# Optimization experiments

Measured on AMD Instinct MI355X. Metric: run time of the kernel, lower is better.

Reference implementation:

```python
import jax, jax.numpy as jnp
import numpy as np

N_SRC = 50000
N_DST = 50000
E = 400000
D_IN = 256
D_OUT = 256


def setup_inputs() -> dict:
    key = jax.random.key(0)
    k1, k2, k3, k4, k5 = jax.random.split(key, 5)
    src_feats = jax.random.normal(k1, (N_SRC, D_IN), dtype=jnp.float32)
    edge_feats = jax.random.normal(k2, (E, D_IN), dtype=jnp.float32)
    src_idx = jax.random.randint(k3, (E,), 0, N_SRC, dtype=jnp.int32)
    dst_idx = jax.random.randint(k4, (E,), 0, N_DST, dtype=jnp.int32)
    # xavier_uniform over [2*in_feat, out_feat] (transposed init in torch, same bound)
    fan_in, fan_out = 2 * D_IN, D_OUT
    bound = np.sqrt(6.0 / (fan_in + fan_out))
    weights = jax.random.uniform(k5, (2 * D_IN, D_OUT), dtype=jnp.float32,
                                 minval=-bound, maxval=bound)
    h_bias = jnp.zeros((D_OUT,), dtype=jnp.float32)
    return {"src_feats": src_feats, "edge_feats": edge_feats,
            "src_idx": src_idx, "dst_idx": dst_idx,
            "weights": weights, "h_bias": h_bias, "num_dst": N_DST}


def reference(src_feats, edge_feats, src_idx, dst_idx, weights, h_bias, num_dst):
    # edge_feat_mp_op == 'concat':
    #   m = concat([src_h, e_h], -1) @ W  ==  src_h @ W[:D] + e_h @ W[D:]
    d = src_feats.shape[1]
    m = src_feats[src_idx] @ weights[:d] + edge_feats @ weights[d:]  # [E, D_OUT]
    # in-degree normalization: norm = in_deg(dst)^{-0.5}, applied per edge (e_mul_v)
    deg = jax.ops.segment_sum(jnp.ones((m.shape[0],), jnp.float32), dst_idx,
                              num_segments=num_dst)
    norm = jnp.where(deg > 0, jax.lax.rsqrt(jnp.maximum(deg, 1.0)), 0.0)
    h = jax.ops.segment_sum(m * norm[dst_idx][:, None], dst_idx,
                            num_segments=num_dst)  # [N_DST, D_OUT]
    return h + h_bias
```

## Files before the change

### kernel.cpp

```cpp
#include <hip/hip_runtime.h>

typedef __attribute__((ext_vector_type(8))) short bf16x8;
typedef __attribute__((ext_vector_type(4))) float f32x4;

#define D_IN 256
#define D_OUT 256
#define KDIM 512
#define GM 64
#define G_ROWS 8
#define CHUNK 2
#define IDCAP 128
#define SCAN_BLOCKS 256

static __device__ __forceinline__ unsigned short f2bf(float f) {
    union { float f; unsigned int u; } x; x.f = f;
    unsigned int r = (x.u + 0x7FFFu + ((x.u >> 16) & 1u)) >> 16;
    return (unsigned short)r;
}

#define GLOAD16(gp, lp) __builtin_amdgcn_global_load_lds(                    \
    (const __attribute__((address_space(1))) void*)(gp),                     \
    (__attribute__((address_space(3))) void*)(lp), 16, 0, 0)

__global__ void zero_wfrag_kernel(int* __restrict__ deg, int n, int zblocks,
                                  const float* __restrict__ W, unsigned short* __restrict__ wf) {
    int b = blockIdx.x;
    if (b < zblocks) {
        int i = b * 256 + threadIdx.x;
        if (i < n) deg[i] = 0;
    } else {
        int t = (b - zblocks) * 256 + threadIdx.x;
        if (t < 16 * 16 * 64) {
            int l  = t & 63;
            int kk = (t >> 6) & 15;
            int nt = t >> 10;
            int c  = nt * 16 + (l & 15);
            int kb = kk * 32 + (l >> 4) * 8;
            union { unsigned short u[8]; uint4 v; } pk;
#pragma unroll
            for (int j = 0; j < 8; ++j) pk.u[j] = f2bf(W[(size_t)(kb + j) * D_OUT + c]);
            *reinterpret_cast<uint4*>(&wf[(size_t)t * 8]) = pk.v;
        }
    }
}

__global__ void count_kernel(const int* __restrict__ dst, int* __restrict__ deg, int E) {
    int e = blockIdx.x * 256 + threadIdx.x;
    if (e < E) atomicAdd(&deg[dst[e]], 1);
}

__global__ void scan_part_kernel(const int* __restrict__ deg, int* __restrict__ part, int n) {
    __shared__ int red[256];
    int b = blockIdx.x, t = threadIdx.x;
    int per = (n + SCAN_BLOCKS - 1) / SCAN_BLOCKS;
    int lo = b * per;
    int hi = lo + per; if (hi > n) hi = n;
    int s = 0;
    for (int i = lo + t; i < hi; i += 256) s += deg[i];
    red[t] = s;
    __syncthreads();
    for (int o = 128; o > 0; o >>= 1) {
        if (t < o) red[t] += red[t + o];
        __syncthreads();
    }
    if (t == 0) part[b] = red[0];
}

__global__ void scan_emit_kernel(const int* __restrict__ deg, const int* __restrict__ part,
                                 int* __restrict__ offsets, int* __restrict__ cursor,
                                 float* __restrict__ norm, int n) {
    int b = blockIdx.x, t = threadIdx.x;
    int per = (n + SCAN_BLOCKS - 1) / SCAN_BLOCKS;
    int lo = b * per;
    int hi = lo + per; if (hi > n) hi = n;
    int v = 0;
    for (int i = t; i < b; i += 64) v += part[i];
#pragma unroll
    for (int o = 32; o > 0; o >>= 1) v += __shfl_down(v, o);
    int base = __shfl(v, 0);
    int sub = (per + 63) / 64;
    int llo = lo + t * sub;
    int lhi = llo + sub;
    if (lhi > hi) lhi = hi;
    if (llo > hi) llo = hi;
    int s = 0;
    for (int i = llo; i < lhi; ++i) s += deg[i];
    int incl = s;
#pragma unroll
    for (int o = 1; o < 64; o <<= 1) { int u = __shfl_up(incl, o); if (t >= o) incl += u; }
    int run = base + incl - s;
    for (int i = llo; i < lhi; ++i) {
        int d = deg[i];
        offsets[i] = run; cursor[i] = run;
        norm[i] = (d > 0) ? rsqrtf((float)d) : 0.0f;
        run += d;
    }
    if (b == SCAN_BLOCKS - 1 && t == 63) offsets[n] = base + incl;
}

__global__ void scatter_kernel(const int* __restrict__ dst, const int* __restrict__ src_idx,
                               int* __restrict__ cursor, int2* __restrict__ rec, int E) {
    int e = blockIdx.x * 256 + threadIdx.x;
    if (e < E) {
        int p = atomicAdd(&cursor[dst[e]], 1);
        rec[p] = make_int2(e, src_idx[e]);
    }
}

__global__ __launch_bounds__(256) void agg_kernel(
    const float* __restrict__ src_feats,
    const float* __restrict__ edge_feats,
    const int2* __restrict__ rec,
    const int* __restrict__ offsets,
    unsigned short* __restrict__ agg,
    int n_dst)
{
    __shared__ __align__(16) float fb[4][2][CHUNK][KDIM];
    __shared__ __align__(16) int2 idb[4][IDCAP + 128];

    const int wv = threadIdx.x >> 6;
    const int ln = threadIdx.x & 63;
    const int rowbase = (blockIdx.x * 4 + wv) * G_ROWS;

    int off_l;
    {
        int k = (ln <= G_ROWS) ? ln : G_ROWS;
        int i = rowbase + k;
        if (i > n_dst) i = n_dst;
        off_l = offsets[i];
    }
    const int s  = __shfl(off_l, 0);
    const int nE = __shfl(off_l, G_ROWS) - s;

    float4 a0 = make_float4(0.f, 0.f, 0.f, 0.f);
    float4 a1 = make_float4(0.f, 0.f, 0.f, 0.f);
    int curRow = 0;
    int curEnd = __shfl(off_l, 1) - s;

    auto flush = [&]() {
        int gr = rowbase + curRow;
        if (gr < n_dst) {
            ushort4 p0, p1;
            p0.x = f2bf(a0.x); p0.y = f2bf(a0.y); p0.z = f2bf(a0.z); p0.w = f2bf(a0.w);
            p1.x = f2bf(a1.x); p1.y = f2bf(a1.y); p1.z = f2bf(a1.z); p1.w = f2bf(a1.w);
            *reinterpret_cast<ushort4*>(&agg[(size_t)gr * KDIM + ln * 4]) = p0;
            *reinterpret_cast<ushort4*>(&agg[(size_t)gr * KDIM + D_IN + ln * 4]) = p1;
        }
        a0 = make_float4(0.f, 0.f, 0.f, 0.f);
        a1 = make_float4(0.f, 0.f, 0.f, 0.f);
    };

    for (int g0 = 0; g0 < nE; g0 += IDCAP) {
        int segN = nE - g0; if (segN > IDCAP) segN = IDCAP;
        const int sg = s + g0;
        const int base16 = sg & ~1;
        const int extra = sg - base16;
        const int idops = ((segN + extra) * 8 + 1023) >> 10;
        for (int o = 0; o < idops; ++o)
            GLOAD16((const char*)(rec + base16) + o * 1024 + ln * 16,
                    (char*)&idb[wv][0] + o * 1024);
        asm volatile("s_waitcnt vmcnt(0)" ::: "memory");
        __builtin_amdgcn_sched_barrier(0);

        const int nCh = (segN + CHUNK - 1) / CHUNK;

        auto issue = [&](int ci) {
            int buf = ci & 1;
            int e0 = ci * CHUNK;
#pragma unroll
            for (int t = 0; t < CHUNK; ++t) {
                int j = e0 + t;
                int sid = 0, eid = 0;
                if (j < segN) { int2 v = idb[wv][j + extra]; eid = v.x; sid = v.y; }
                float* lp = &fb[wv][buf][t][0];
                GLOAD16(src_feats  + (size_t)sid * D_IN + ln * 4, lp);
                GLOAD16(edge_feats + (size_t)eid * D_IN + ln * 4, lp + D_IN);
            }
        };

        issue(0); issue(1);
        for (int ci = 0; ci < nCh; ++ci) {
            asm volatile("s_waitcnt vmcnt(4)" ::: "memory");
            __builtin_amdgcn_sched_barrier(0);
            int buf = ci & 1;
            int e0 = ci * CHUNK;
#pragma unroll
            for (int t = 0; t < CHUNK; ++t) {
                int j = e0 + t;
                if (j >= segN) break;
                int ja = g0 + j;
                while (ja >= curEnd) {
                    flush();
                    ++curRow;
                    curEnd = __shfl(off_l, curRow + 1) - s;
                }
                float4 v0 = *reinterpret_cast<const float4*>(&fb[wv][buf][t][ln * 4]);
                float4 v1 = *reinterpret_cast<const float4*>(&fb[wv][buf][t][D_IN + ln * 4]);
                a0.x += v0.x; a0.y += v0.y; a0.z += v0.z; a0.w += v0.w;
                a1.x += v1.x; a1.y += v1.y; a1.z += v1.z; a1.w += v1.w;
            }
            issue(ci + 2);
        }
        asm volatile("s_waitcnt vmcnt(0)" ::: "memory");
        __builtin_amdgcn_sched_barrier(0);
    }
    while (curRow < G_ROWS) { flush(); ++curRow; }
}

__global__ __launch_bounds__(256) void gemm_kernel(
    const unsigned short* __restrict__ agg,
    const unsigned short* __restrict__ wfrag,
    const float* __restrict__ norm,
    const float* __restrict__ bias,
    float* __restrict__ out,
    int n_dst)
{
    __shared__ __align__(16) unsigned short As[GM * KDIM];

    const int wv = threadIdx.x >> 6;
    const int ln = threadIdx.x & 63;
    const int lrow = ln & 15;
    const int lgrp = ln >> 4;
    const int base = blockIdx.x * GM;

    for (int r = wv; r < GM; r += 4) {
        int gr = base + r; if (gr >= n_dst) gr = n_dst - 1;
        GLOAD16(agg + (size_t)gr * KDIM + (size_t)((ln ^ (r & 7)) * 8),
                (char*)As + r * 1024);
    }
    asm volatile("s_waitcnt vmcnt(0)" ::: "memory");
    __syncthreads();

    f32x4 acc[4][4];
#pragma unroll
    for (int m = 0; m < 4; ++m)
#pragma unroll
        for (int n = 0; n < 4; ++n) acc[m][n] = (f32x4)(0.0f);

#pragma unroll
    for (int kk = 0; kk < 16; ++kk) {
        bf16x8 A[4];
#pragma unroll
        for (int m = 0; m < 4; ++m) {
            int r = m * 16 + lrow;
            int g = (kk * 4 + lgrp) ^ (r & 7);
            A[m] = *reinterpret_cast<const bf16x8*>((const char*)As + r * 1024 + g * 16);
        }
#pragma unroll
        for (int n = 0; n < 4; ++n) {
            int nt = wv * 4 + n;
            bf16x8 B = *reinterpret_cast<const bf16x8*>(&wfrag[(((size_t)nt * 16 + kk) * 64 + ln) * 8]);
#pragma unroll
            for (int m = 0; m < 4; ++m)
                acc[m][n] = __builtin_amdgcn_mfma_f32_16x16x32_bf16(A[m], B, acc[m][n], 0, 0, 0);
        }
    }

    float bias_r[4];
#pragma unroll
    for (int n = 0; n < 4; ++n) bias_r[n] = bias[wv * 64 + n * 16 + lrow];

#pragma unroll
    for (int m = 0; m < 4; ++m) {
#pragma unroll
        for (int j = 0; j < 4; ++j) {
            int r = base + m * 16 + lgrp * 4 + j;
            if (r < n_dst) {
                float nv = norm[r];
#pragma unroll
                for (int n = 0; n < 4; ++n)
                    out[(size_t)r * D_OUT + wv * 64 + n * 16 + lrow] = acc[m][n][j] * nv + bias_r[n];
            }
        }
    }
}

extern "C" void kernel_launch(void* const* d_in, const int* in_sizes, int n_in,
                              void* d_out, int out_size, void* d_ws, size_t ws_size,
                              hipStream_t stream) {
    const float* src_feats  = (const float*)d_in[0];
    const float* edge_feats = (const float*)d_in[1];
    const int*   src_idx    = (const int*)d_in[2];
    const int*   dst_idx    = (const int*)d_in[3];
    const float* weights    = (const float*)d_in[4];
    const float* h_bias     = (const float*)d_in[5];

    const int E     = in_sizes[2];
    const int n_dst = out_size / D_OUT;
    float* out = (float*)d_out;

    char* ws = (char*)d_ws;
    size_t agg_bytes = (size_t)n_dst * KDIM * 2;
    unsigned short* agg   = (unsigned short*)ws;
    unsigned short* wfrag = (unsigned short*)(ws + agg_bytes);
    int2* rec     = (int2*)(ws + agg_bytes + 262144);
    char* after_rec = ws + agg_bytes + 262144 + (size_t)E * 8 + 2048;
    int*  deg     = (int*)after_rec;
    int*  offsets = deg + n_dst;
    int*  cursor  = offsets + n_dst + 1;
    float* norm   = (float*)(cursor + n_dst);
    int*  part    = (int*)(norm + n_dst);

    const int CB = (E + 255) / 256;
    const int ZB = (n_dst + 255) / 256;

    zero_wfrag_kernel<<<ZB + 64, 256, 0, stream>>>(deg, n_dst, ZB, weights, wfrag);
    count_kernel<<<CB, 256, 0, stream>>>(dst_idx, deg, E);
    scan_part_kernel<<<SCAN_BLOCKS, 256, 0, stream>>>(deg, part, n_dst);
    scan_emit_kernel<<<SCAN_BLOCKS, 64, 0, stream>>>(deg, part, offsets, cursor, norm, n_dst);
    scatter_kernel<<<CB, 256, 0, stream>>>(dst_idx, src_idx, cursor, rec, E);

    agg_kernel<<<(n_dst + 4 * G_ROWS - 1) / (4 * G_ROWS), 256, 0, stream>>>(
        src_feats, edge_feats, rec, offsets, agg, n_dst);
    gemm_kernel<<<(n_dst + GM - 1) / GM, 256, 0, stream>>>(
        agg, wfrag, norm, h_bias, out, n_dst);
}
```

Measured before the change: 237.8 us.

## Deepen agg gather pipeline to 4 single-edge buffers and split GEMM A-load by K half

The aggregation kernel stops processing edges in chunks of two with double buffering and instead processes one edge per step with a 4-slot ring buffer, keeping three edges of gathers in flight. The GEMM kernel loads the A tile in two K halves and starts MFMAs on the first half while the second half is still arriving. Both changes aim to hide global-memory latency. The cost is more waitcnt/loop overhead per edge in the gather and an extra barrier plus a changed LDS swizzle layout in the GEMM.

```diff
diff --git a/kernel.cpp b/kernel.cpp
--- a/kernel.cpp
+++ b/kernel.cpp
@@ -8,7 +8,6 @@
 #define KDIM 512
 #define GM 64
 #define G_ROWS 8
-#define CHUNK 2
 #define IDCAP 128
 #define SCAN_BLOCKS 256
 
@@ -115,7 +114,7 @@
     unsigned short* __restrict__ agg,
     int n_dst)
 {
-    __shared__ __align__(16) float fb[4][2][CHUNK][KDIM];
+    __shared__ __align__(16) float fb[4][4][KDIM];
     __shared__ __align__(16) int2 idb[4][IDCAP + 128];
 
     const int wv = threadIdx.x >> 6;
@@ -162,44 +161,31 @@
         asm volatile("s_waitcnt vmcnt(0)" ::: "memory");
         __builtin_amdgcn_sched_barrier(0);
 
-        const int nCh = (segN + CHUNK - 1) / CHUNK;
-
         auto issue = [&](int ci) {
-            int buf = ci & 1;
-            int e0 = ci * CHUNK;
-#pragma unroll
-            for (int t = 0; t < CHUNK; ++t) {
-                int j = e0 + t;
-                int sid = 0, eid = 0;
-                if (j < segN) { int2 v = idb[wv][j + extra]; eid = v.x; sid = v.y; }
-                float* lp = &fb[wv][buf][t][0];
-                GLOAD16(src_feats  + (size_t)sid * D_IN + ln * 4, lp);
-                GLOAD16(edge_feats + (size_t)eid * D_IN + ln * 4, lp + D_IN);
-            }
+            int buf = ci & 3;
+            int sid = 0, eid = 0;
+            if (ci < segN) { int2 v = idb[wv][ci + extra]; eid = v.x; sid = v.y; }
+            float* lp = &fb[wv][buf][0];
+            GLOAD16(src_feats  + (size_t)sid * D_IN + ln * 4, lp);
+            GLOAD16(edge_feats + (size_t)eid * D_IN + ln * 4, lp + D_IN);
         };
 
-        issue(0); issue(1);
-        for (int ci = 0; ci < nCh; ++ci) {
+        issue(0); issue(1); issue(2);
+        for (int ci = 0; ci < segN; ++ci) {
             asm volatile("s_waitcnt vmcnt(4)" ::: "memory");
             __builtin_amdgcn_sched_barrier(0);
-            int buf = ci & 1;
-            int e0 = ci * CHUNK;
-#pragma unroll
-            for (int t = 0; t < CHUNK; ++t) {
-                int j = e0 + t;
-                if (j >= segN) break;
-                int ja = g0 + j;
-                while (ja >= curEnd) {
-                    flush();
-                    ++curRow;
-                    curEnd = __shfl(off_l, curRow + 1) - s;
-                }
-                float4 v0 = *reinterpret_cast<const float4*>(&fb[wv][buf][t][ln * 4]);
-                float4 v1 = *reinterpret_cast<const float4*>(&fb[wv][buf][t][D_IN + ln * 4]);
-                a0.x += v0.x; a0.y += v0.y; a0.z += v0.z; a0.w += v0.w;
-                a1.x += v1.x; a1.y += v1.y; a1.z += v1.z; a1.w += v1.w;
+            int buf = ci & 3;
+            int ja = g0 + ci;
+            while (ja >= curEnd) {
+                flush();
+                ++curRow;
+                curEnd = __shfl(off_l, curRow + 1) - s;
             }
-            issue(ci + 2);
+            float4 v0 = *reinterpret_cast<const float4*>(&fb[wv][buf][ln * 4]);
+            float4 v1 = *reinterpret_cast<const float4*>(&fb[wv][buf][D_IN + ln * 4]);
+            a0.x += v0.x; a0.y += v0.y; a0.z += v0.z; a0.w += v0.w;
+            a1.x += v1.x; a1.y += v1.y; a1.z += v1.z; a1.w += v1.w;
+            issue(ci + 3);
         }
         asm volatile("s_waitcnt vmcnt(0)" ::: "memory");
         __builtin_amdgcn_sched_barrier(0);
@@ -215,7 +201,7 @@
     float* __restrict__ out,
     int n_dst)
 {
-    __shared__ __align__(16) unsigned short As[GM * KDIM];
+    __shared__ __align__(16) unsigned short As[2 * GM * 256];
 
     const int wv = threadIdx.x >> 6;
     const int ln = threadIdx.x & 63;
@@ -223,13 +209,18 @@
     const int lgrp = ln >> 4;
     const int base = blockIdx.x * GM;
 
-    for (int r = wv; r < GM; r += 4) {
-        int gr = base + r; if (gr >= n_dst) gr = n_dst - 1;
-        GLOAD16(agg + (size_t)gr * KDIM + (size_t)((ln ^ (r & 7)) * 8),
-                (char*)As + r * 1024);
-    }
-    asm volatile("s_waitcnt vmcnt(0)" ::: "memory");
-    __syncthreads();
+#pragma unroll
+    for (int h = 0; h < 2; ++h) {
+#pragma unroll
+        for (int q = 0; q < 8; ++q) {
+            int p = q * 4 + wv;
+            int r = 2 * p + (ln >> 5);
+            int gr = base + r; if (gr >= n_dst) gr = n_dst - 1;
+            int sg = (ln & 31) ^ (r & 7);
+            GLOAD16(agg + (size_t)gr * KDIM + h * 256 + sg * 8,
+                    (char*)As + h * 32768 + p * 1024);
+        }
+    }
 
     f32x4 acc[4][4];
 #pragma unroll
@@ -237,14 +228,41 @@
 #pragma unroll
         for (int n = 0; n < 4; ++n) acc[m][n] = (f32x4)(0.0f);
 
-#pragma unroll
-    for (int kk = 0; kk < 16; ++kk) {
+    asm volatile("s_waitcnt vmcnt(8)" ::: "memory");
+    __builtin_amdgcn_s_barrier();
+    __builtin_amdgcn_sched_barrier(0);
+
+#pragma unroll
+    for (int kk = 0; kk < 8; ++kk) {
         bf16x8 A[4];
 #pragma unroll
         for (int m = 0; m < 4; ++m) {
             int r = m * 16 + lrow;
             int g = (kk * 4 + lgrp) ^ (r & 7);
-            A[m] = *reinterpret_cast<const bf16x8*>((const char*)As + r * 1024 + g * 16);
+            A[m] = *reinterpret_cast<const bf16x8*>((const char*)As + r * 512 + g * 16);
+        }
+#pragma unroll
+        for (int n = 0; n < 4; ++n) {
+            int nt = wv * 4 + n;
+            bf16x8 B = *reinterpret_cast<const bf16x8*>(&wfrag[(((size_t)nt * 16 + kk) * 64 + ln) * 8]);
+#pragma unroll
+            for (int m = 0; m < 4; ++m)
+                acc[m][n] = __builtin_amdgcn_mfma_f32_16x16x32_bf16(A[m], B, acc[m][n], 0, 0, 0);
+        }
+    }
+
+    asm volatile("s_waitcnt vmcnt(0)" ::: "memory");
+    __builtin_amdgcn_s_barrier();
+    __builtin_amdgcn_sched_barrier(0);
+
+#pragma unroll
+    for (int kk = 8; kk < 16; ++kk) {
+        bf16x8 A[4];
+#pragma unroll
+        for (int m = 0; m < 4; ++m) {
+            int r = m * 16 + lrow;
+            int g = ((kk - 8) * 4 + lgrp) ^ (r & 7);
+            A[m] = *reinterpret_cast<const bf16x8*>((const char*)As + 32768 + r * 512 + g * 16);
         }
 #pragma unroll
         for (int n = 0; n < 4; ++n) {
```

New measurement: 242.2 us. Within noise of the previous version (+1.9%).
